# Performance work log

Hardware: AMD Instinct MI355X
Metric: run time of the kernel (lower is better)

## Reference

```python
import jax, jax.numpy as jnp
import numpy as np

N = 100000        # nodes
E = 3200000       # random edges (avg degree 32); self-loops added in reference
IN, HID, HEADS, OUT = 10, 32, 2, 4
NEG_SLOPE = 0.2   # PyG GATConv default leaky_relu slope


def setup_inputs() -> dict:
    key = jax.random.key(0)
    ks = jax.random.split(key, 16)
    s = 0.1
    return {
        "x": jax.random.normal(ks[0], (N, IN), jnp.float32),
        "edge_index": jax.random.randint(ks[1], (2, E), 0, N),
        "W1": jax.random.normal(ks[2], (IN, HEADS * HID), jnp.float32) * s,
        "a1s": jax.random.normal(ks[3], (HEADS, HID), jnp.float32) * s,
        "a1d": jax.random.normal(ks[4], (HEADS, HID), jnp.float32) * s,
        "b1": jnp.zeros((HEADS * HID,), jnp.float32),
        "W2": jax.random.normal(ks[5], (HEADS * HID, HEADS * HID), jnp.float32) * s,
        "a2s": jax.random.normal(ks[6], (HEADS, HID), jnp.float32) * s,
        "a2d": jax.random.normal(ks[7], (HEADS, HID), jnp.float32) * s,
        "b2": jnp.zeros((HEADS * HID,), jnp.float32),
        "W3": jax.random.normal(ks[8], (HEADS * HID, OUT), jnp.float32) * s,
        "a3s": jax.random.normal(ks[9], (1, OUT), jnp.float32) * s,
        "a3d": jax.random.normal(ks[10], (1, OUT), jnp.float32) * s,
        "b3": jnp.zeros((OUT,), jnp.float32),
    }


def gat_layer(x, src, dst, W, a_src, a_dst, b, concat):
    """One PyG-style GATConv (shared src/dst linear, self-loops already in src/dst)."""
    heads, oc = a_src.shape
    h = (x @ W).reshape(-1, heads, oc)                    # [N, H, C]
    asc = jnp.einsum('nhc,hc->nh', h, a_src)              # [N, H]
    adc = jnp.einsum('nhc,hc->nh', h, a_dst)              # [N, H]
    e = jax.nn.leaky_relu(asc[src] + adc[dst], NEG_SLOPE) # [Etot, H]
    m = jax.ops.segment_max(e, dst, num_segments=N)       # segment softmax over dst
    ex = jnp.exp(e - m[dst])
    z = jax.ops.segment_sum(ex, dst, num_segments=N)
    alpha = ex / z[dst]                                   # [Etot, H]
    out = jax.ops.segment_sum(h[src] * alpha[:, :, None], dst, num_segments=N)
    out = out.reshape(-1, heads * oc) if concat else out.mean(axis=1)
    return out + b


def reference(x, edge_index, W1, a1s, a1d, b1, W2, a2s, a2d, b2, W3, a3s, a3d, b3):
    loops = jnp.arange(N)
    src = jnp.concatenate([edge_index[0], loops])
    dst = jnp.concatenate([edge_index[1], loops])
    h = jax.nn.relu(gat_layer(x, src, dst, W1, a1s, a1d, b1, True))
    h = jax.nn.relu(gat_layer(h, src, dst, W2, a2s, a2d, b2, True))
    h = gat_layer(h, src, dst, W3, a3s, a3d, b3, False)
    return jax.nn.sigmoid(h) * 100.0
```

## Files before the change

kernel.cpp:

```cpp
#include <hip/hip_runtime.h>
#include <hip/hip_bf16.h>
#include <math.h>

#define NEG_SLOPE 0.2f
#define PSHIFT 8
#define PSIZE 256
#define NPARTS_MAX 392
#define B1 768
#define CELL_CAP 32
#define LCSR_CAP 10240

typedef int vint2 __attribute__((ext_vector_type(2)));
typedef int vint4 __attribute__((ext_vector_type(4)));
typedef short bf16x8 __attribute__((ext_vector_type(8)));
typedef float floatx4 __attribute__((ext_vector_type(4)));

__device__ __forceinline__ float lrelu(float v) { return fmaxf(v, NEG_SLOPE * v); }

__device__ __forceinline__ unsigned short f2bf(float f) {
    unsigned int b = __float_as_uint(f);
    b += 0x7fffu + ((b >> 16) & 1u);
    return (unsigned short)(b >> 16);
}
__device__ __forceinline__ float bf2f(unsigned short u) {
    return __uint_as_float((unsigned int)u << 16);
}

__global__ void k_part(const int* __restrict__ src, const int* __restrict__ dst, int E,
                       int* __restrict__ pairs, int* __restrict__ pcnt,
                       int* __restrict__ ptot, int nparts) {
    __shared__ int stage[NPARTS_MAX * CELL_CAP];
    __shared__ int lcnt[NPARTS_MAX];
    int tid = threadIdx.x, blk = blockIdx.x;
    for (int i = tid; i < nparts; i += 256) lcnt[i] = 0;
    __syncthreads();
    int per = ((E + B1 * 4 - 1) / (B1 * 4)) * 4;
    int s = blk * per, e = min(E, s + per);
    bool al = ((E & 3) == 0);
    for (int i0 = s + tid * 4; i0 < e; i0 += 1024) {
        int dv[4], sv[4], nv;
        if (al && i0 + 4 <= e) {
            vint4 d4 = __builtin_nontemporal_load((const vint4*)(dst + i0));
            vint4 s4 = __builtin_nontemporal_load((const vint4*)(src + i0));
            dv[0] = d4.x; dv[1] = d4.y; dv[2] = d4.z; dv[3] = d4.w;
            sv[0] = s4.x; sv[1] = s4.y; sv[2] = s4.z; sv[3] = s4.w;
            nv = 4;
        } else {
            nv = min(4, e - i0);
            for (int k = 0; k < nv; ++k) {
                dv[k] = __builtin_nontemporal_load(dst + i0 + k);
                sv[k] = __builtin_nontemporal_load(src + i0 + k);
            }
        }
        for (int k = 0; k < nv; ++k) {
            int p = dv[k] >> PSHIFT;
            int pos = atomicAdd(&lcnt[p], 1);
            if (pos < CELL_CAP)
                stage[p * CELL_CAP + pos] = (sv[k] << PSHIFT) | (dv[k] & (PSIZE - 1));
        }
    }
    __syncthreads();
    for (int p = tid; p < nparts; p += 256) {
        int tgt = min(lcnt[p], CELL_CAP);
        int* gp = pairs + ((size_t)p * B1 + blk) * CELL_CAP;
        const int* sp = &stage[p * CELL_CAP];
        int j = 0;
        for (; j + 4 <= tgt; j += 4)
            *(vint4*)(gp + j) = *(const vint4*)(sp + j);
        for (; j < tgt; ++j) gp[j] = sp[j];
        pcnt[p * B1 + blk] = tgt;
        atomicAdd(&ptot[p], tgt);
    }
}

__global__ void k_pscan(const int* __restrict__ ptot, int* __restrict__ pbase,
                        int* __restrict__ row, int nparts, int N) {
    __shared__ int sh[512];
    int tid = threadIdx.x;
    int v = (tid < nparts) ? ptot[tid] : 0;
    sh[tid] = v;
    __syncthreads();
    for (int off = 1; off < 512; off <<= 1) {
        int t = (tid >= off) ? sh[tid - off] : 0;
        __syncthreads();
        sh[tid] += t;
        __syncthreads();
    }
    if (tid < nparts) pbase[tid] = sh[tid] - v;
    if (tid == nparts - 1) row[N] = sh[tid];
}

__global__ void k_scat2(const int* __restrict__ pairs, const int* __restrict__ pcnt,
                        const int* __restrict__ pbase, int* __restrict__ row,
                        int* __restrict__ csr, int N) {
    __shared__ int lcsr[LCSR_CAP];
    __shared__ int lhist[PSIZE], lcur[PSIZE];
    __shared__ int stot;
    int part = blockIdx.x;
    int lo = part << PSHIFT;
    int npart = min(PSIZE, N - lo);
    int tid = threadIdx.x;
    int wid = tid >> 6, lane = tid & 63;
    for (int i = tid; i < PSIZE; i += 1024) lhist[i] = 0;
    __syncthreads();
    for (int c = wid; c < B1; c += 16) {
        int nb = pcnt[part * B1 + c];
        if (lane < nb) {
            int v = __builtin_nontemporal_load(pairs + ((size_t)part * B1 + c) * CELL_CAP + lane);
            atomicAdd(&lhist[v & (PSIZE - 1)], 1);
        }
    }
    __syncthreads();
    if (tid < PSIZE) lcur[tid] = lhist[tid];
    __syncthreads();
    for (int off = 1; off < PSIZE; off <<= 1) {
        int t = 0;
        if (tid < PSIZE && tid >= off) t = lcur[tid - off];
        __syncthreads();
        if (tid < PSIZE) lcur[tid] += t;
        __syncthreads();
    }
    int pb = pbase[part];
    if (tid == PSIZE - 1) stot = lcur[tid];
    if (tid < npart) row[lo + tid] = pb + lcur[tid] - lhist[tid];
    if (tid < PSIZE) lcur[tid] -= lhist[tid];
    __syncthreads();
    for (int c = wid; c < B1; c += 16) {
        int nb = pcnt[part * B1 + c];
        if (lane < nb) {
            int v = __builtin_nontemporal_load(pairs + ((size_t)part * B1 + c) * CELL_CAP + lane);
            int pos = atomicAdd(&lcur[v & (PSIZE - 1)], 1);
            if (pos < LCSR_CAP) lcsr[pos] = (unsigned)v >> PSHIFT;
        }
    }
    __syncthreads();
    int T = min(stot, LCSR_CAP);
    for (int i = tid; i < T; i += 1024)
        csr[pb + i] = lcsr[i];
}

__global__ void k_lin1(const float* __restrict__ x, const float* __restrict__ W,
                       const float* __restrict__ as_, const float* __restrict__ ad_,
                       unsigned short* __restrict__ hb, float* __restrict__ asc,
                       float* __restrict__ adc, int N) {
    __shared__ float sW[10 * 64];
    int tid = threadIdx.x;
    for (int i = tid; i < 640; i += 256) sW[i] = W[i];
    __syncthreads();
    int wid = tid >> 6, lane = tid & 63;
    int n = blockIdx.x * 4 + wid;
    if (n >= N) return;
    float acc = 0.f;
#pragma unroll
    for (int k = 0; k < 10; ++k) acc += x[n * 10 + k] * sW[k * 64 + lane];
    hb[(size_t)n * 64 + lane] = f2bf(acc);
    int head = lane >> 5, cc = lane & 31;
    float rs = acc * as_[lane];
    float rd = acc * ad_[lane];
#pragma unroll
    for (int m = 16; m >= 1; m >>= 1) {
        rs += __shfl_xor(rs, m, 64);
        rd += __shfl_xor(rd, m, 64);
    }
    if (cc == 0) { asc[n * 2 + head] = rs; adc[n * 2 + head] = rd; }
}

__global__ void k_lin2(const float* __restrict__ yin, const float* __restrict__ W,
                       const float* __restrict__ as_, const float* __restrict__ ad_,
                       unsigned short* __restrict__ hb, float* __restrict__ asc,
                       float* __restrict__ adc, int N) {
    __shared__ unsigned short sW[64 * 64];
    int tid = threadIdx.x;
    for (int i = tid; i < 4096; i += 256) sW[i] = f2bf(W[i]);
    __syncthreads();
    int wid = tid >> 6, lane = tid & 63;
    int quad = lane >> 4, col = lane & 15;
    bf16x8 bfr[4][2];
#pragma unroll
    for (int blk = 0; blk < 4; ++blk)
#pragma unroll
        for (int kh = 0; kh < 2; ++kh)
#pragma unroll
            for (int j = 0; j < 8; ++j)
                bfr[blk][kh][j] = (short)sW[(kh * 32 + quad * 8 + j) * 64 + blk * 16 + col];
    float asv[4], adv[4];
#pragma unroll
    for (int blk = 0; blk < 4; ++blk) {
        asv[blk] = as_[blk * 16 + col];
        adv[blk] = ad_[blk * 16 + col];
    }
    int tile = blockIdx.x * 4 + wid;
    int nb = tile * 16;
    if (nb >= N) return;
    int mrow = nb + col; if (mrow >= N) mrow = N - 1;
    const float* yr = yin + (size_t)mrow * 64;
    bf16x8 afr[2];
#pragma unroll
    for (int kh = 0; kh < 2; ++kh) {
        const float4* p = (const float4*)(yr + kh * 32 + quad * 8);
        float4 u0 = p[0], u1 = p[1];
        afr[kh][0] = (short)f2bf(u0.x); afr[kh][1] = (short)f2bf(u0.y);
        afr[kh][2] = (short)f2bf(u0.z); afr[kh][3] = (short)f2bf(u0.w);
        afr[kh][4] = (short)f2bf(u1.x); afr[kh][5] = (short)f2bf(u1.y);
        afr[kh][6] = (short)f2bf(u1.z); afr[kh][7] = (short)f2bf(u1.w);
    }
    floatx4 acc[4];
#pragma unroll
    for (int blk = 0; blk < 4; ++blk) {
        acc[blk][0] = 0.f; acc[blk][1] = 0.f; acc[blk][2] = 0.f; acc[blk][3] = 0.f;
        acc[blk] = __builtin_amdgcn_mfma_f32_16x16x32_bf16(afr[0], bfr[blk][0], acc[blk], 0, 0, 0);
        acc[blk] = __builtin_amdgcn_mfma_f32_16x16x32_bf16(afr[1], bfr[blk][1], acc[blk], 0, 0, 0);
    }
#pragma unroll
    for (int r = 0; r < 4; ++r) {
        int m = nb + quad * 4 + r;
        if (m < N) {
#pragma unroll
            for (int blk = 0; blk < 4; ++blk)
                hb[(size_t)m * 64 + blk * 16 + col] = f2bf(acc[blk][r]);
        }
    }
    float s0[4], s1[4], d0[4], d1[4];
#pragma unroll
    for (int r = 0; r < 4; ++r) {
        s0[r] = acc[0][r] * asv[0] + acc[1][r] * asv[1];
        s1[r] = acc[2][r] * asv[2] + acc[3][r] * asv[3];
        d0[r] = acc[0][r] * adv[0] + acc[1][r] * adv[1];
        d1[r] = acc[2][r] * adv[2] + acc[3][r] * adv[3];
    }
#pragma unroll
    for (int mask = 8; mask >= 1; mask >>= 1) {
#pragma unroll
        for (int r = 0; r < 4; ++r) {
            s0[r] += __shfl_xor(s0[r], mask, 64);
            s1[r] += __shfl_xor(s1[r], mask, 64);
            d0[r] += __shfl_xor(d0[r], mask, 64);
            d1[r] += __shfl_xor(d1[r], mask, 64);
        }
    }
    if (col < 4) {
        int m = nb + quad * 4 + col;
        if (m < N) {
            float vs0 = col == 0 ? s0[0] : col == 1 ? s0[1] : col == 2 ? s0[2] : s0[3];
            float vs1 = col == 0 ? s1[0] : col == 1 ? s1[1] : col == 2 ? s1[2] : s1[3];
            float vd0 = col == 0 ? d0[0] : col == 1 ? d0[1] : col == 2 ? d0[2] : d0[3];
            float vd1 = col == 0 ? d1[0] : col == 1 ? d1[1] : col == 2 ? d1[2] : d1[3];
            asc[m * 2 + 0] = vs0; asc[m * 2 + 1] = vs1;
            adc[m * 2 + 0] = vd0; adc[m * 2 + 1] = vd1;
        }
    }
}

__global__ void k_agg(const unsigned short* __restrict__ hb, const float* __restrict__ asc,
                      const float* __restrict__ adc, const int* __restrict__ row,
                      const int* __restrict__ csr_src, const float* __restrict__ bias,
                      float* __restrict__ yout, int N, int do_relu) {
    __shared__ vint2 tbl[4][64];
    int tid = threadIdx.x;
    int wid = tid >> 6, lane = tid & 63;
    int n = blockIdx.x * 4 + wid;
    if (n >= N) return;
    int s = row[n], e = row[n + 1];
    int head = lane >> 5, sub = lane & 31;
    int half = lane >> 5;
    int cpair = lane & 31;
    int hL = (cpair >> 4) & 1;
    float2 ad = ((const float2*)adc)[n];
    float adch = head ? ad.y : ad.x;
    float2 asf = ((const float2*)asc)[n];
    float p_self_h = __expf(lrelu((head ? asf.y : asf.x) + adch));
    float zl = (sub == 0) ? p_self_h : 0.f;
    float acc0 = 0.f, acc1 = 0.f;
    const unsigned int* hb32 = (const unsigned int*)hb;
    for (int base = s; base < e; base += 32) {
        int cnt = e - base; if (cnt > 32) cnt = 32;
        int idx = base + sub;
        int srcv = 0;
        float p_l = 0.f;
        if (idx < e) {
            srcv = csr_src[idx];
            p_l = __expf(lrelu(asc[(size_t)srcv * 2 + head] + adch));
        }
        zl += p_l;
        vint2 ent; ent.x = srcv; ent.y = __float_as_int(p_l);
        tbl[wid][(head << 5) | sub] = ent;
        __builtin_amdgcn_wave_barrier();
        int tb = hL << 5;
        int cnt2 = (cnt + 1) & ~1;
#pragma unroll 4
        for (int j = half; j < cnt2; j += 2) {
            vint2 t = tbl[wid][tb | j];
            unsigned int pk = hb32[(size_t)t.x * 32 + cpair];
            float p = __int_as_float(t.y);
            acc0 += p * __uint_as_float(pk << 16);
            acc1 += p * __uint_as_float(pk & 0xffff0000u);
        }
        __builtin_amdgcn_wave_barrier();
    }
    acc0 += __shfl_xor(acc0, 32, 64);
    acc1 += __shfl_xor(acc1, 32, 64);
#pragma unroll
    for (int msk = 16; msk >= 1; msk >>= 1) zl += __shfl_xor(zl, msk, 64);
    float zo = __shfl_xor(zl, 32, 64);
    float zneed = (hL == (lane >> 5)) ? zl : zo;
    float adcm = hL ? ad.y : ad.x;
    float p_self_my = __expf(lrelu((hL ? asf.y : asf.x) + adcm));
    unsigned int pks = hb32[(size_t)n * 32 + cpair];
    acc0 += p_self_my * __uint_as_float(pks << 16);
    acc1 += p_self_my * __uint_as_float(pks & 0xffff0000u);
    float inv = 1.f / zneed;
    float2 bv = ((const float2*)bias)[cpair];
    float y0 = acc0 * inv + bv.x;
    float y1 = acc1 * inv + bv.y;
    if (do_relu) { y0 = fmaxf(y0, 0.f); y1 = fmaxf(y1, 0.f); }
    if (lane < 32) {
        float2 o; o.x = y0; o.y = y1;
        ((float2*)yout)[(size_t)n * 32 + cpair] = o;
    }
}

__global__ void k_lin3(const float* __restrict__ yin, const float* __restrict__ W3,
                       const float* __restrict__ a3s, const float* __restrict__ a3d,
                       float* __restrict__ h3, float* __restrict__ asc3, float* __restrict__ adc3,
                       int N) {
    __shared__ float sW[256];
    int tid = threadIdx.x;
    sW[tid] = W3[tid];
    __syncthreads();
    int t = blockIdx.x * 256 + tid;
    int n = t >> 2, c = t & 3;
    if (n >= N) return;
    float acc = 0.f;
#pragma unroll
    for (int k = 0; k < 64; ++k) acc += yin[(size_t)n * 64 + k] * sW[k * 4 + c];
    h3[(size_t)n * 4 + c] = acc;
    float rs = acc * a3s[c], rd = acc * a3d[c];
    rs += __shfl_xor(rs, 1, 64); rs += __shfl_xor(rs, 2, 64);
    rd += __shfl_xor(rd, 1, 64); rd += __shfl_xor(rd, 2, 64);
    if (c == 0) { asc3[n] = rs; adc3[n] = rd; }
}

__global__ void k_agg3(const float* __restrict__ h3, const float* __restrict__ asc3,
                       const float* __restrict__ adc3, const int* __restrict__ row,
                       const int* __restrict__ csr_src, const float* __restrict__ b3,
                       float* __restrict__ out, int N) {
    int tid = threadIdx.x;
    int wid = tid >> 6, lane = tid & 63;
    int n = blockIdx.x * 4 + wid;
    if (n >= N) return;
    int s = row[n], e = row[n + 1];
    float adcn = adc3[n];
    float p_self = __expf(lrelu(asc3[n] + adcn));
    int c = lane & 3, jg = lane >> 2;
    float num = (jg == 0) ? p_self * h3[(size_t)n * 4 + c] : 0.f;
    float den = (jg == 0) ? p_self : 0.f;
    for (int base = s; base < e; base += 16) {
        int idx = base + jg;
        if (idx < e) {
            int src = csr_src[idx];
            float p = __expf(lrelu(asc3[src] + adcn));
            num += p * h3[(size_t)src * 4 + c];
            den += p;
        }
    }
#pragma unroll
    for (int mask = 4; mask <= 32; mask <<= 1) {
        num += __shfl_xor(num, mask, 64);
        den += __shfl_xor(den, mask, 64);
    }
    if (lane < 4) {
        float v = num / den + b3[c];
        out[n * 4 + c] = 100.f / (1.f + __expf(-v));
    }
}

extern "C" void kernel_launch(void* const* d_in, const int* in_sizes, int n_in,
                              void* d_out, int out_size, void* d_ws, size_t ws_size,
                              hipStream_t stream) {
    const float* x   = (const float*)d_in[0];
    const int*   ei  = (const int*)d_in[1];
    const float* W1  = (const float*)d_in[2];
    const float* a1s = (const float*)d_in[3];
    const float* a1d = (const float*)d_in[4];
    const float* b1  = (const float*)d_in[5];
    const float* W2  = (const float*)d_in[6];
    const float* a2s = (const float*)d_in[7];
    const float* a2d = (const float*)d_in[8];
    const float* b2  = (const float*)d_in[9];
    const float* W3  = (const float*)d_in[10];
    const float* a3s = (const float*)d_in[11];
    const float* a3d = (const float*)d_in[12];
    const float* b3  = (const float*)d_in[13];
    float* out = (float*)d_out;

    const int N = in_sizes[0] / 10;
    const int E = in_sizes[1] / 2;
    const int* esrc = ei;
    const int* edst = ei + E;
    const int nparts = (N + PSIZE - 1) >> PSHIFT;

    char* ws = (char*)d_ws;
    size_t off = 0;
    auto alloc = [&](size_t bytes) {
        void* p = ws + off;
        off = (off + bytes + 255) & ~(size_t)255;
        return p;
    };
    int*   row   = (int*)alloc((size_t)(N + 1) * sizeof(int));
    int*   ptot  = (int*)alloc(NPARTS_MAX * sizeof(int));
    int*   pbase = (int*)alloc(NPARTS_MAX * sizeof(int));
    int*   pcnt  = (int*)alloc((size_t)NPARTS_MAX * B1 * sizeof(int));
    int*   csr   = (int*)alloc((size_t)E * sizeof(int));
    unsigned short* hb = (unsigned short*)alloc((size_t)N * 64 * sizeof(unsigned short));
    float* y     = (float*)alloc((size_t)N * 64 * sizeof(float));
    float* l3scr = (float*)alloc((size_t)N * 6 * sizeof(float));
    float* asc   = (float*)alloc((size_t)N * 2 * sizeof(float));
    float* adc   = (float*)alloc((size_t)N * 2 * sizeof(float));
    float* h3   = l3scr;
    float* asc3 = l3scr + (size_t)N * 4;
    float* adc3 = l3scr + (size_t)N * 5;
    int* pairs = (int*)hb;

    (void)hipMemsetAsync(ptot, 0, NPARTS_MAX * sizeof(int), stream);

    const int nw = (N + 3) / 4;
    const int tiles = (N + 15) / 16;

    k_part<<<B1, 256, 0, stream>>>(esrc, edst, E, pairs, pcnt, ptot, nparts);
    k_pscan<<<1, 512, 0, stream>>>(ptot, pbase, row, nparts, N);
    k_scat2<<<nparts, 1024, 0, stream>>>(pairs, pcnt, pbase, row, csr, N);

    k_lin1<<<nw, 256, 0, stream>>>(x, W1, a1s, a1d, hb, asc, adc, N);
    k_agg<<<nw, 256, 0, stream>>>(hb, asc, adc, row, csr, b1, y, N, 1);
    k_lin2<<<(tiles + 3) / 4, 256, 0, stream>>>(y, W2, a2s, a2d, hb, asc, adc, N);
    k_agg<<<nw, 256, 0, stream>>>(hb, asc, adc, row, csr, b2, y, N, 1);
    k_lin3<<<(N * 4 + 255) / 256, 256, 0, stream>>>(y, W3, a3s, a3d, h3, asc3, adc3, N);
    k_agg3<<<nw, 256, 0, stream>>>(h3, asc3, adc3, row, csr, b3, out, N);
}
```

Before: 441.3 us.

## Compact partition buckets via atomic offsets and widen aggregation gathers to 8 bytes

The partition kernel now reserves a contiguous slot range per partition with an atomic add and writes edges into a dense per-partition segment, so the scatter kernel reads one contiguous array and no longer needs a per-block count table or a pass over mostly empty cells. Separately, the aggregation kernel gathers 4 bf16 channels per lane (8-byte loads) with four neighbor streams per head instead of two, which halves the number of gather instructions per edge. The cost is an added cross-lane reduction stage, only 16 lanes doing the store, and atomic contention on the per-partition counters. Partitions are also hard-capped at PCAP entries.

Result: faster. 373.4 us (-15.4%).

```diff
diff --git a/kernel.cpp b/kernel.cpp
--- a/kernel.cpp
+++ b/kernel.cpp
@@ -8,6 +8,7 @@
 #define NPARTS_MAX 392
 #define B1 768
 #define CELL_CAP 32
+#define PCAP 10240
 #define LCSR_CAP 10240
 
 typedef int vint2 __attribute__((ext_vector_type(2)));
@@ -27,8 +28,7 @@
 }
 
 __global__ void k_part(const int* __restrict__ src, const int* __restrict__ dst, int E,
-                       int* __restrict__ pairs, int* __restrict__ pcnt,
-                       int* __restrict__ ptot, int nparts) {
+                       int* __restrict__ pairs, int* __restrict__ ptot, int nparts) {
     __shared__ int stage[NPARTS_MAX * CELL_CAP];
     __shared__ int lcnt[NPARTS_MAX];
     int tid = threadIdx.x, blk = blockIdx.x;
@@ -62,14 +62,12 @@
     __syncthreads();
     for (int p = tid; p < nparts; p += 256) {
         int tgt = min(lcnt[p], CELL_CAP);
-        int* gp = pairs + ((size_t)p * B1 + blk) * CELL_CAP;
+        if (tgt == 0) continue;
+        int base = atomicAdd(&ptot[p], tgt);
+        if (base + tgt > PCAP) tgt = max(0, PCAP - base);
+        int* gp = pairs + (size_t)p * PCAP + base;
         const int* sp = &stage[p * CELL_CAP];
-        int j = 0;
-        for (; j + 4 <= tgt; j += 4)
-            *(vint4*)(gp + j) = *(const vint4*)(sp + j);
-        for (; j < tgt; ++j) gp[j] = sp[j];
-        pcnt[p * B1 + blk] = tgt;
-        atomicAdd(&ptot[p], tgt);
+        for (int j = 0; j < tgt; ++j) gp[j] = sp[j];
     }
 }
 
@@ -77,7 +75,7 @@
                         int* __restrict__ row, int nparts, int N) {
     __shared__ int sh[512];
     int tid = threadIdx.x;
-    int v = (tid < nparts) ? ptot[tid] : 0;
+    int v = (tid < nparts) ? min(ptot[tid], PCAP) : 0;
     sh[tid] = v;
     __syncthreads();
     for (int off = 1; off < 512; off <<= 1) {
@@ -90,26 +88,21 @@
     if (tid == nparts - 1) row[N] = sh[tid];
 }
 
-__global__ void k_scat2(const int* __restrict__ pairs, const int* __restrict__ pcnt,
+__global__ void k_scat2(const int* __restrict__ pairs, const int* __restrict__ ptot,
                         const int* __restrict__ pbase, int* __restrict__ row,
                         int* __restrict__ csr, int N) {
     __shared__ int lcsr[LCSR_CAP];
     __shared__ int lhist[PSIZE], lcur[PSIZE];
-    __shared__ int stot;
     int part = blockIdx.x;
     int lo = part << PSHIFT;
     int npart = min(PSIZE, N - lo);
     int tid = threadIdx.x;
-    int wid = tid >> 6, lane = tid & 63;
+    int cnt = min(ptot[part], PCAP);
+    const int* seg = pairs + (size_t)part * PCAP;
     for (int i = tid; i < PSIZE; i += 1024) lhist[i] = 0;
     __syncthreads();
-    for (int c = wid; c < B1; c += 16) {
-        int nb = pcnt[part * B1 + c];
-        if (lane < nb) {
-            int v = __builtin_nontemporal_load(pairs + ((size_t)part * B1 + c) * CELL_CAP + lane);
-            atomicAdd(&lhist[v & (PSIZE - 1)], 1);
-        }
-    }
+    for (int i = tid; i < cnt; i += 1024)
+        atomicAdd(&lhist[__builtin_nontemporal_load(&seg[i]) & (PSIZE - 1)], 1);
     __syncthreads();
     if (tid < PSIZE) lcur[tid] = lhist[tid];
     __syncthreads();
@@ -121,21 +114,16 @@
         __syncthreads();
     }
     int pb = pbase[part];
-    if (tid == PSIZE - 1) stot = lcur[tid];
     if (tid < npart) row[lo + tid] = pb + lcur[tid] - lhist[tid];
     if (tid < PSIZE) lcur[tid] -= lhist[tid];
     __syncthreads();
-    for (int c = wid; c < B1; c += 16) {
-        int nb = pcnt[part * B1 + c];
-        if (lane < nb) {
-            int v = __builtin_nontemporal_load(pairs + ((size_t)part * B1 + c) * CELL_CAP + lane);
-            int pos = atomicAdd(&lcur[v & (PSIZE - 1)], 1);
-            if (pos < LCSR_CAP) lcsr[pos] = (unsigned)v >> PSHIFT;
-        }
-    }
-    __syncthreads();
-    int T = min(stot, LCSR_CAP);
-    for (int i = tid; i < T; i += 1024)
+    for (int i = tid; i < cnt; i += 1024) {
+        int v = __builtin_nontemporal_load(&seg[i]);
+        int pos = atomicAdd(&lcur[v & (PSIZE - 1)], 1);
+        if (pos < LCSR_CAP) lcsr[pos] = (unsigned)v >> PSHIFT;
+    }
+    __syncthreads();
+    for (int i = tid; i < cnt; i += 1024)
         csr[pb + i] = lcsr[i];
 }
 
@@ -262,16 +250,16 @@
     if (n >= N) return;
     int s = row[n], e = row[n + 1];
     int head = lane >> 5, sub = lane & 31;
-    int half = lane >> 5;
-    int cpair = lane & 31;
-    int hL = (cpair >> 4) & 1;
+    int chq = lane & 15;
+    int hq = chq >> 3;
+    int jo = lane >> 4;
     float2 ad = ((const float2*)adc)[n];
     float adch = head ? ad.y : ad.x;
     float2 asf = ((const float2*)asc)[n];
     float p_self_h = __expf(lrelu((head ? asf.y : asf.x) + adch));
     float zl = (sub == 0) ? p_self_h : 0.f;
-    float acc0 = 0.f, acc1 = 0.f;
-    const unsigned int* hb32 = (const unsigned int*)hb;
+    float a0 = 0.f, a1 = 0.f, a2 = 0.f, a3 = 0.f;
+    const vint2* hb64 = (const vint2*)hb;
     for (int base = s; base < e; base += 32) {
         int cnt = e - base; if (cnt > 32) cnt = 32;
         int idx = base + sub;
@@ -285,37 +273,49 @@
         vint2 ent; ent.x = srcv; ent.y = __float_as_int(p_l);
         tbl[wid][(head << 5) | sub] = ent;
         __builtin_amdgcn_wave_barrier();
-        int tb = hL << 5;
-        int cnt2 = (cnt + 1) & ~1;
-#pragma unroll 4
-        for (int j = half; j < cnt2; j += 2) {
+        int tb = hq << 5;
+#pragma unroll 2
+        for (int j = jo; j < cnt; j += 4) {
             vint2 t = tbl[wid][tb | j];
-            unsigned int pk = hb32[(size_t)t.x * 32 + cpair];
+            vint2 pk = hb64[(size_t)t.x * 16 + chq];
             float p = __int_as_float(t.y);
-            acc0 += p * __uint_as_float(pk << 16);
-            acc1 += p * __uint_as_float(pk & 0xffff0000u);
+            unsigned int pa = (unsigned int)pk.x, pb = (unsigned int)pk.y;
+            a0 += p * __uint_as_float(pa << 16);
+            a1 += p * __uint_as_float(pa & 0xffff0000u);
+            a2 += p * __uint_as_float(pb << 16);
+            a3 += p * __uint_as_float(pb & 0xffff0000u);
         }
         __builtin_amdgcn_wave_barrier();
     }
-    acc0 += __shfl_xor(acc0, 32, 64);
-    acc1 += __shfl_xor(acc1, 32, 64);
+    a0 += __shfl_xor(a0, 16, 64); a1 += __shfl_xor(a1, 16, 64);
+    a2 += __shfl_xor(a2, 16, 64); a3 += __shfl_xor(a3, 16, 64);
+    a0 += __shfl_xor(a0, 32, 64); a1 += __shfl_xor(a1, 32, 64);
+    a2 += __shfl_xor(a2, 32, 64); a3 += __shfl_xor(a3, 32, 64);
 #pragma unroll
     for (int msk = 16; msk >= 1; msk >>= 1) zl += __shfl_xor(zl, msk, 64);
     float zo = __shfl_xor(zl, 32, 64);
-    float zneed = (hL == (lane >> 5)) ? zl : zo;
-    float adcm = hL ? ad.y : ad.x;
-    float p_self_my = __expf(lrelu((hL ? asf.y : asf.x) + adcm));
-    unsigned int pks = hb32[(size_t)n * 32 + cpair];
-    acc0 += p_self_my * __uint_as_float(pks << 16);
-    acc1 += p_self_my * __uint_as_float(pks & 0xffff0000u);
+    float zneed = (hq == head) ? zl : zo;
+    float adcm = hq ? ad.y : ad.x;
+    float p_self_my = __expf(lrelu((hq ? asf.y : asf.x) + adcm));
+    vint2 pks = hb64[(size_t)n * 16 + chq];
+    unsigned int sa = (unsigned int)pks.x, sb = (unsigned int)pks.y;
+    a0 += p_self_my * __uint_as_float(sa << 16);
+    a1 += p_self_my * __uint_as_float(sa & 0xffff0000u);
+    a2 += p_self_my * __uint_as_float(sb << 16);
+    a3 += p_self_my * __uint_as_float(sb & 0xffff0000u);
     float inv = 1.f / zneed;
-    float2 bv = ((const float2*)bias)[cpair];
-    float y0 = acc0 * inv + bv.x;
-    float y1 = acc1 * inv + bv.y;
-    if (do_relu) { y0 = fmaxf(y0, 0.f); y1 = fmaxf(y1, 0.f); }
-    if (lane < 32) {
-        float2 o; o.x = y0; o.y = y1;
-        ((float2*)yout)[(size_t)n * 32 + cpair] = o;
+    float4 bv = ((const float4*)bias)[chq];
+    float y0 = a0 * inv + bv.x;
+    float y1 = a1 * inv + bv.y;
+    float y2 = a2 * inv + bv.z;
+    float y3 = a3 * inv + bv.w;
+    if (do_relu) {
+        y0 = fmaxf(y0, 0.f); y1 = fmaxf(y1, 0.f);
+        y2 = fmaxf(y2, 0.f); y3 = fmaxf(y3, 0.f);
+    }
+    if (lane < 16) {
+        float4 o; o.x = y0; o.y = y1; o.z = y2; o.w = y3;
+        ((float4*)yout)[(size_t)n * 16 + chq] = o;
     }
 }
 
@@ -409,7 +409,6 @@
     int*   row   = (int*)alloc((size_t)(N + 1) * sizeof(int));
     int*   ptot  = (int*)alloc(NPARTS_MAX * sizeof(int));
     int*   pbase = (int*)alloc(NPARTS_MAX * sizeof(int));
-    int*   pcnt  = (int*)alloc((size_t)NPARTS_MAX * B1 * sizeof(int));
     int*   csr   = (int*)alloc((size_t)E * sizeof(int));
     unsigned short* hb = (unsigned short*)alloc((size_t)N * 64 * sizeof(unsigned short));
     float* y     = (float*)alloc((size_t)N * 64 * sizeof(float));
@@ -426,9 +425,9 @@
     const int nw = (N + 3) / 4;
     const int tiles = (N + 15) / 16;
 
-    k_part<<<B1, 256, 0, stream>>>(esrc, edst, E, pairs, pcnt, ptot, nparts);
+    k_part<<<B1, 256, 0, stream>>>(esrc, edst, E, pairs, ptot, nparts);
     k_pscan<<<1, 512, 0, stream>>>(ptot, pbase, row, nparts, N);
-    k_scat2<<<nparts, 1024, 0, stream>>>(pairs, pcnt, pbase, row, csr, N);
+    k_scat2<<<nparts, 1024, 0, stream>>>(pairs, ptot, pbase, row, csr, N);
 
     k_lin1<<<nw, 256, 0, stream>>>(x, W1, a1s, a1d, hb, asc, adc, N);
     k_agg<<<nw, 256, 0, stream>>>(hb, asc, adc, row, csr, b1, y, N, 1);
```
